# Performance work log

Measured on AMD Instinct MI355X. Metric: run time of the kernel, lower is better.

## Reference

```python
import jax, jax.numpy as jnp
import numpy as np
from math import ceil

SCALE = (0.25, 0.25)
IM_SIZE = (1080, 1920)
KERNEL_WIDTH = 4.0


def _cubic(x):
    absx = np.abs(x)
    absx2 = absx * absx
    absx3 = absx2 * absx
    return ((1.5 * absx3 - 2.5 * absx2 + 1) * (absx <= 1)
            + (-0.5 * absx3 + 2.5 * absx2 - 4 * absx + 2) * ((1 < absx) * (absx <= 2)))


def _contributions(in_length, out_length, scale):
    # MATLAB-style imresize contributions (matches the torch module's numpy code)
    if scale < 1:
        h = lambda v: scale * _cubic(scale * v)
        kernel_width = KERNEL_WIDTH / scale
    else:
        h = _cubic
        kernel_width = KERNEL_WIDTH
    x = np.arange(1, out_length + 1).astype(np.float64)
    u = x / scale + 0.5 * (1 - 1 / scale)
    left = np.floor(u - kernel_width / 2)
    P = int(ceil(kernel_width)) + 2
    ind = np.expand_dims(left, axis=1) + np.arange(P) - 1
    indices = ind.astype(np.int32)
    weights = h(np.expand_dims(u, axis=1) - indices - 1)
    weights = weights / np.sum(weights, axis=1, keepdims=True)
    aux = np.concatenate((np.arange(in_length), np.arange(in_length - 1, -1, -1))).astype(np.int32)
    indices = aux[np.mod(indices, aux.size)]
    keep = np.nonzero(np.any(weights, axis=0))[0]
    return weights[:, keep].astype(np.float32), indices[:, keep].astype(np.int64)


def setup_inputs() -> dict:
    key = jax.random.key(0)
    B, C = 8, 3
    H, W = IM_SIZE
    x = jax.random.normal(key, (B, C, H, W), dtype=jnp.float32)
    out_h = int(ceil(SCALE[0] * H))
    out_w = int(ceil(SCALE[1] * W))
    w_h, idx_h = _contributions(H, out_h, SCALE[0])
    w_w, idx_w = _contributions(W, out_w, SCALE[1])
    return {
        "x": x,
        "w_h": jnp.asarray(w_h), "idx_h": jnp.asarray(idx_h),
        "w_w": jnp.asarray(w_w), "idx_w": jnp.asarray(idx_w),
    }


def reference(x, w_h, idx_h, w_w, idx_w):
    # x: [B, C, H, W] -> work in [B, H, W, C] like the torch transpose dance
    xb = jnp.transpose(x, (0, 2, 3, 1))
    # scale is equal along both axes -> argsort order is [0, 1]: resize H then W
    # gather rows: [B, outH, P, W, C], contract over P with weights [outH, P]
    g = xb[:, idx_h, :, :]
    xb = jnp.einsum("op,bopwc->bowc", w_h, g)
    # gather cols: [B, outH, outW, P, C]
    g = xb[:, :, idx_w, :]
    xb = jnp.einsum("op,bhopc->bhoc", w_w, g)
    return jnp.transpose(xb, (0, 3, 1, 2))
```

## Files before the change

kernel.cpp:

```cpp
#include <hip/hip_runtime.h>

namespace {

constexpr int H  = 1080;
constexpr int W  = 1920;
constexpr int OH = 270;
constexpr int OW = 480;
constexpr int KT = 16;
constexpr int G  = 2;
constexpr int NCHUNK = 133;
constexpr int ROWS = 4 * G + 12;
constexpr int VSTRIDE = 1032;

constexpr int EDGE_FULL = 4 * OW;
constexpr int EDGE_TOT  = EDGE_FULL + (OH - 4) * 4;
constexpr int EDGE_YS   = 6;

__global__ __launch_bounds__(256, 4) void bicubic_fused(
    const float* __restrict__ x,
    const float* __restrict__ wh,
    const int*   __restrict__ ih,
    const float* __restrict__ ww,
    const int*   __restrict__ iw,
    float*       __restrict__ out)
{
    __shared__ float vbuf[G * VSTRIDE];

    const int tid = threadIdx.x;
    const int bx  = blockIdx.x;
    const int by  = blockIdx.y;
    const int bc  = blockIdx.z;

    if (by < EDGE_YS) {
        const int idx = (by * 2 + bx) * 256 + tid;
        if (idx >= EDGE_TOT) return;

        int oh, ow;
        if (idx < EDGE_FULL) {
            int q = idx / OW;
            ow = idx - q * OW;
            oh = (q < 2) ? q : OH - 4 + q;
        } else {
            int t = idx - EDGE_FULL;
            int q = t & 3;
            oh = 2 + (t >> 2);
            ow = (q < 2) ? q : OW - 4 + q;
        }

        const float* __restrict__ img = x + (size_t)bc * ((size_t)H * W);

        float wt[KT];
        __builtin_memcpy(wt, ww + (size_t)ow * KT, sizeof(wt));
        int ir[KT];
        __builtin_memcpy(ir, iw + (size_t)ow * KT, sizeof(ir));

        bool fastc = true;
        #pragma unroll
        for (int k = 1; k < KT; ++k) fastc = fastc && (ir[k] == ir[0] + k);
        const int i0 = ir[0];

        float acc = 0.0f;
        #pragma unroll
        for (int kh = 0; kh < KT; ++kh) {
            const int   r = ih[oh * KT + kh];
            const float w = wh[oh * KT + kh];
            const float* row = img + (size_t)r * W;
            float h = 0.0f;
            if (fastc) {
                float v[KT];
                __builtin_memcpy(v, row + i0, sizeof(v));
                #pragma unroll
                for (int k = 0; k < KT; ++k) h = fmaf(v[k], wt[k], h);
            } else {
                #pragma unroll
                for (int k = 0; k < KT; ++k) h = fmaf(row[ir[k]], wt[k], h);
            }
            acc = fmaf(w, h, acc);
        }
        out[((size_t)bc * OH + oh) * OW + ow] = acc;
        return;
    }

    const int owb = bx ? 254 : 2;
    const int Nw  = bx ? 224 : 252;
    const int c0  = 4 * owb - 8;
    const int oh0 = 2 + G * (by - EDGE_YS);
    const int r0  = 4 * oh0 - 6;

    float wr[KT];
    __builtin_memcpy(wr, wh + (size_t)oh0 * KT, sizeof(wr));

    int c = c0 + 4 * tid;
    if (c > W - 4) c = W - 4;
    const float* __restrict__ p =
        x + ((size_t)bc * H + (size_t)r0) * W + c;

    float v[ROWS][4];
    #pragma unroll
    for (int r = 0; r < ROWS; ++r)
        __builtin_memcpy(v[r], p + (size_t)r * W, 16);

    __builtin_amdgcn_sched_barrier(0);

    float a0[4] = {0.f, 0.f, 0.f, 0.f};
    float a1[4] = {0.f, 0.f, 0.f, 0.f};
    #pragma unroll
    for (int r = 0; r < 16; ++r) {
        const float w = wr[r];
        #pragma unroll
        for (int cc = 0; cc < 4; ++cc) a0[cc] = fmaf(w, v[r][cc], a0[cc]);
    }
    #pragma unroll
    for (int r = 4; r < ROWS; ++r) {
        const float w = wr[r - 4];
        #pragma unroll
        for (int cc = 0; cc < 4; ++cc) a1[cc] = fmaf(w, v[r][cc], a1[cc]);
    }

    __builtin_memcpy(&vbuf[0 * VSTRIDE + 4 * tid + 2], a0, 16);
    __builtin_memcpy(&vbuf[1 * VSTRIDE + 4 * tid + 2], a1, 16);
    __syncthreads();

    if (tid < Nw) {
        const int ow = owb + tid;
        float wt[KT];
        __builtin_memcpy(wt, ww + (size_t)ow * KT, sizeof(wt));
        float* __restrict__ obase =
            out + ((size_t)bc * OH + oh0) * OW + ow;
        #pragma unroll
        for (int t = 0; t < G; ++t) {
            float vv[KT];
            __builtin_memcpy(vv, &vbuf[t * VSTRIDE + 4 * tid + 4], sizeof(vv));
            float s0 = 0.f, s1 = 0.f;
            #pragma unroll
            for (int k = 0; k < KT; k += 2) {
                s0 = fmaf(vv[k],     wt[k],     s0);
                s1 = fmaf(vv[k + 1], wt[k + 1], s1);
            }
            obase[(size_t)t * OW] = s0 + s1;
        }
    }
}

__global__ __launch_bounds__(256) void bicubic_generic(
    const float* __restrict__ x,
    const float* __restrict__ wh,
    const int*   __restrict__ ih,
    const float* __restrict__ ww,
    const int*   __restrict__ iw,
    float*       __restrict__ out,
    int Kh, int Kw, int total)
{
    int t = blockIdx.x * blockDim.x + threadIdx.x;
    if (t >= total) return;
    int ow = t % OW;
    int oh = (t / OW) % OH;
    int bc = t / (OW * OH);
    const float* img = x + (size_t)bc * ((size_t)H * W);
    float acc = 0.0f;
    for (int kh = 0; kh < Kh; ++kh) {
        const int   r = ih[oh * Kh + kh];
        const float w = wh[oh * Kh + kh];
        const float* row = img + (size_t)r * W;
        float h = 0.0f;
        for (int k = 0; k < Kw; ++k)
            h = fmaf(row[iw[ow * Kw + k]], ww[ow * Kw + k], h);
        acc = fmaf(w, h, acc);
    }
    out[t] = acc;
}

}

extern "C" void kernel_launch(void* const* d_in, const int* in_sizes, int n_in,
                              void* d_out, int out_size, void* d_ws, size_t ws_size,
                              hipStream_t stream) {
    const float* x  = (const float*)d_in[0];
    const float* wh = (const float*)d_in[1];
    const int*   ih = (const int*)d_in[2];
    const float* ww = (const float*)d_in[3];
    const int*   iw = (const int*)d_in[4];
    float*       out = (float*)d_out;

    const int BC = in_sizes[0] / (H * W);
    const int Kh = in_sizes[1] / OH;
    const int Kw = in_sizes[3] / OW;

    if (Kh == KT && Kw == KT) {
        dim3 grid(2, EDGE_YS + NCHUNK, BC);
        bicubic_fused<<<grid, 256, 0, stream>>>(x, wh, ih, ww, iw, out);
    } else {
        int total = BC * OH * OW;
        bicubic_generic<<<(total + 255) / 256, 256, 0, stream>>>(
            x, wh, ih, ww, iw, out, Kh, Kw, total);
    }
}
```

Measured before the change: 324.7 us.

## Process 14 output rows per block with rolling pipelined row loads

Each interior block now produces 14 output rows instead of 2, streaming 68 input rows through an 8-deep register ring of inline-asm global loads with explicit vmcnt waits. Four rotating vertical accumulators let each loaded input row feed several overlapping output rows, and the horizontal pass runs per row through a double-buffered LDS strip. This cuts redundant re-reads of overlapping input rows and launches far fewer blocks. The cost is fewer blocks for latency hiding, a barrier per output row, and fragile hand-written asm offset arithmetic.

```diff
diff --git a/kernel.cpp b/kernel.cpp
--- a/kernel.cpp
+++ b/kernel.cpp
@@ -7,14 +7,99 @@
 constexpr int OH = 270;
 constexpr int OW = 480;
 constexpr int KT = 16;
-constexpr int G  = 2;
-constexpr int NCHUNK = 133;
-constexpr int ROWS = 4 * G + 12;
+constexpr int GSEG = 14;
+constexpr int NSEG = 19;
+constexpr int RPB  = 4 * GSEG + 12;
+constexpr int DEPTH = 8;
 constexpr int VSTRIDE = 1032;
 
 constexpr int EDGE_FULL = 4 * OW;
 constexpr int EDGE_TOT  = EDGE_FULL + (OH - 4) * 4;
 constexpr int EDGE_YS   = 6;
+
+typedef float vf4 __attribute__((ext_vector_type(4)));
+
+__device__ __forceinline__ void fma4(vf4& a, float w, const vf4& v) {
+    #pragma unroll
+    for (int i = 0; i < 4; ++i) a[i] = fmaf(w, v[i], a[i]);
+}
+
+__device__ __forceinline__ void issue_load(vf4& dst, unsigned& voff,
+                                           const float* pbase) {
+    asm volatile("global_load_dwordx4 %0, %1, %2\n\t"
+                 "v_add_u32 %1, 0x1e00, %1"
+                 : "=&v"(dst), "+v"(voff)
+                 : "s"(pbase));
+}
+
+template<int N> __device__ __forceinline__ void wait_vmcnt() {
+    static_assert(N >= 0 && N <= 7, "");
+    if constexpr      (N == 0) asm volatile("s_waitcnt vmcnt(0)");
+    else if constexpr (N == 1) asm volatile("s_waitcnt vmcnt(1)");
+    else if constexpr (N == 2) asm volatile("s_waitcnt vmcnt(2)");
+    else if constexpr (N == 3) asm volatile("s_waitcnt vmcnt(3)");
+    else if constexpr (N == 4) asm volatile("s_waitcnt vmcnt(4)");
+    else if constexpr (N == 5) asm volatile("s_waitcnt vmcnt(5)");
+    else if constexpr (N == 6) asm volatile("s_waitcnt vmcnt(6)");
+    else                       asm volatile("s_waitcnt vmcnt(7)");
+    __builtin_amdgcn_sched_barrier(0);
+}
+
+__device__ __forceinline__ void do_close(int J, vf4& acc, float* vb,
+    int tid, int Nw, const float (&wt)[KT], float* obase)
+{
+    __builtin_memcpy(vb + (J & 1) * VSTRIDE + 4 * tid + 2, &acc, 16);
+    acc = vf4{0.f, 0.f, 0.f, 0.f};
+    asm volatile("s_waitcnt lgkmcnt(0)" ::: "memory");
+    __builtin_amdgcn_s_barrier();
+    if (tid < Nw) {
+        float vv[KT];
+        __builtin_memcpy(vv, vb + (J & 1) * VSTRIDE + 4 * tid + 4, sizeof(vv));
+        float s0 = 0.f, s1 = 0.f;
+        #pragma unroll
+        for (int k = 0; k < KT; k += 2) {
+            s0 = fmaf(vv[k],     wt[k],     s0);
+            s1 = fmaf(vv[k + 1], wt[k + 1], s1);
+        }
+        obase[(size_t)J * OW] = s0 + s1;
+    }
+}
+
+template<int RR>
+__device__ __forceinline__ void row_step(vf4 (&ring)[DEPTH], vf4 (&A)[4],
+    unsigned& voff, const float* pbase, const float (&wr)[KT],
+    float* vb, int tid, int Nw, const float (&wt)[KT], float* obase)
+{
+    constexpr int OUT = (RPB - 1 - RR) < 7 ? (RPB - 1 - RR) : 7;
+    wait_vmcnt<OUT>();
+    vf4 v = ring[RR & (DEPTH - 1)];
+    if constexpr (RR + DEPTH < RPB)
+        issue_load(ring[RR & (DEPTH - 1)], voff, pbase);
+
+    constexpr int M = RR >> 2, Q = RR & 3;
+    if constexpr (M - 0 >= 0 && M - 0 <= GSEG - 1) fma4(A[(M - 0) & 3], wr[Q +  0], v);
+    if constexpr (M - 1 >= 0 && M - 1 <= GSEG - 1) fma4(A[(M - 1) & 3], wr[Q +  4], v);
+    if constexpr (M - 2 >= 0 && M - 2 <= GSEG - 1) fma4(A[(M - 2) & 3], wr[Q +  8], v);
+    if constexpr (M - 3 >= 0 && M - 3 <= GSEG - 1) fma4(A[(M - 3) & 3], wr[Q + 12], v);
+
+    if constexpr (Q == 3 && M >= 3 && (M - 3) <= GSEG - 1)
+        do_close(M - 3, A[(M - 3) & 3], vb, tid, Nw, wt, obase);
+}
+
+template<int RR> struct RowsT {
+    static __device__ __forceinline__ void run(vf4 (&ring)[DEPTH], vf4 (&A)[4],
+        unsigned& voff, const float* pbase, const float (&wr)[KT],
+        float* vb, int tid, int Nw, const float (&wt)[KT], float* obase)
+    {
+        row_step<RR>(ring, A, voff, pbase, wr, vb, tid, Nw, wt, obase);
+        RowsT<RR + 1>::run(ring, A, voff, pbase, wr, vb, tid, Nw, wt, obase);
+    }
+};
+template<> struct RowsT<RPB> {
+    static __device__ __forceinline__ void run(vf4 (&)[DEPTH], vf4 (&)[4],
+        unsigned&, const float*, const float (&)[KT],
+        float*, int, int, const float (&)[KT], float*) {}
+};
 
 __global__ __launch_bounds__(256, 4) void bicubic_fused(
     const float* __restrict__ x,
@@ -24,7 +109,7 @@
     const int*   __restrict__ iw,
     float*       __restrict__ out)
 {
-    __shared__ float vbuf[G * VSTRIDE];
+    __shared__ float vbuf[2 * VSTRIDE];
 
     const int tid = threadIdx.x;
     const int bx  = blockIdx.x;
@@ -84,62 +169,31 @@
     const int owb = bx ? 254 : 2;
     const int Nw  = bx ? 224 : 252;
     const int c0  = 4 * owb - 8;
-    const int oh0 = 2 + G * (by - EDGE_YS);
+    const int seg = by - EDGE_YS;
+    const int oh0 = 2 + GSEG * seg;
     const int r0  = 4 * oh0 - 6;
 
     float wr[KT];
     __builtin_memcpy(wr, wh + (size_t)oh0 * KT, sizeof(wr));
 
+    const int owc = (owb + tid < OW) ? (owb + tid) : (OW - 1);
+    float wt[KT];
+    __builtin_memcpy(wt, ww + (size_t)owc * KT, sizeof(wt));
+
     int c = c0 + 4 * tid;
     if (c > W - 4) c = W - 4;
-    const float* __restrict__ p =
-        x + ((size_t)bc * H + (size_t)r0) * W + c;
-
-    float v[ROWS][4];
+
+    const float* pbase = x + ((size_t)bc * H + (size_t)r0) * W;
+    unsigned voff = (unsigned)(4 * c);
+
+    vf4 ring[DEPTH];
+    vf4 A[4] = {vf4{0,0,0,0}, vf4{0,0,0,0}, vf4{0,0,0,0}, vf4{0,0,0,0}};
+
     #pragma unroll
-    for (int r = 0; r < ROWS; ++r)
-        __builtin_memcpy(v[r], p + (size_t)r * W, 16);
-
-    __builtin_amdgcn_sched_barrier(0);
-
-    float a0[4] = {0.f, 0.f, 0.f, 0.f};
-    float a1[4] = {0.f, 0.f, 0.f, 0.f};
-    #pragma unroll
-    for (int r = 0; r < 16; ++r) {
-        const float w = wr[r];
-        #pragma unroll
-        for (int cc = 0; cc < 4; ++cc) a0[cc] = fmaf(w, v[r][cc], a0[cc]);
-    }
-    #pragma unroll
-    for (int r = 4; r < ROWS; ++r) {
-        const float w = wr[r - 4];
-        #pragma unroll
-        for (int cc = 0; cc < 4; ++cc) a1[cc] = fmaf(w, v[r][cc], a1[cc]);
-    }
-
-    __builtin_memcpy(&vbuf[0 * VSTRIDE + 4 * tid + 2], a0, 16);
-    __builtin_memcpy(&vbuf[1 * VSTRIDE + 4 * tid + 2], a1, 16);
-    __syncthreads();
-
-    if (tid < Nw) {
-        const int ow = owb + tid;
-        float wt[KT];
-        __builtin_memcpy(wt, ww + (size_t)ow * KT, sizeof(wt));
-        float* __restrict__ obase =
-            out + ((size_t)bc * OH + oh0) * OW + ow;
-        #pragma unroll
-        for (int t = 0; t < G; ++t) {
-            float vv[KT];
-            __builtin_memcpy(vv, &vbuf[t * VSTRIDE + 4 * tid + 4], sizeof(vv));
-            float s0 = 0.f, s1 = 0.f;
-            #pragma unroll
-            for (int k = 0; k < KT; k += 2) {
-                s0 = fmaf(vv[k],     wt[k],     s0);
-                s1 = fmaf(vv[k + 1], wt[k + 1], s1);
-            }
-            obase[(size_t)t * OW] = s0 + s1;
-        }
-    }
+    for (int i = 0; i < DEPTH; ++i) issue_load(ring[i], voff, pbase);
+
+    float* obase = out + ((size_t)bc * OH + oh0) * OW + owb + tid;
+    RowsT<0>::run(ring, A, voff, pbase, wr, vbuf, tid, Nw, wt, obase);
 }
 
 __global__ __launch_bounds__(256) void bicubic_generic(
@@ -187,7 +241,7 @@
     const int Kw = in_sizes[3] / OW;
 
     if (Kh == KT && Kw == KT) {
-        dim3 grid(2, EDGE_YS + NCHUNK, BC);
+        dim3 grid(2, EDGE_YS + NSEG, BC);
         bicubic_fused<<<grid, 256, 0, stream>>>(x, wh, ih, ww, iw, out);
     } else {
         int total = BC * OH * OW;
```

Result: no change. 321.6 us (-0.9%).
